# Optimization experiments

Measured on AMD Instinct MI355X. Metric: run time of the kernel, lower is better.

## Reference

```python
import jax, jax.numpy as jnp
import numpy as np
from jax import lax

RADIUS = 4
SIGMA_1 = 5.0
SIGMA_2 = 1.0


def _gaussian_kernel_3d(radius, sigma):
    x = np.linspace(-radius, radius, 2 * radius + 1)
    xx, yy, zz = np.meshgrid(x, x, x)
    dist2 = xx ** 2 + yy ** 2 + zz ** 2
    k = np.exp(-dist2 / (2.0 * sigma ** 2)).astype(np.float32)
    return jnp.asarray(k)[None, None]  # [O=1, I=1, D, H, W]


def _conv3d_same(x, kernel, radius):
    # x: [B,1,D,H,W], kernel: [1,1,kd,kh,kw]
    pad = [(radius, radius)] * 3
    return lax.conv_general_dilated(
        x, kernel, window_strides=(1, 1, 1), padding=pad,
        dimension_numbers=('NCDHW', 'OIDHW', 'NCDHW'))


def setup_inputs() -> dict:
    key = jax.random.key(0)
    k1, k2 = jax.random.split(key)
    labels = jax.random.uniform(k1, (4, 1, 160, 160, 160), dtype=jnp.float32)
    inputs = jax.random.uniform(k2, (4, 1, 160, 160, 160), dtype=jnp.float32)
    return {"labels": labels, "inputs": inputs}


def reference(labels, inputs):
    kernel = _gaussian_kernel_3d(RADIUS, SIGMA_1)
    num_classes = 2
    p0 = labels[:, 0:1]  # [B,1,D,H,W]
    loss = jnp.float32(0.0)
    for k in range(num_classes):
        class_probs = p0 if k == 0 else 1.0 - p0
        class_mean = (jnp.mean(inputs * class_probs, axis=(2, 3, 4), keepdims=True)
                      / (jnp.mean(class_probs, axis=(2, 3, 4), keepdims=True) + 1e-5))
        diff = jnp.sum((inputs - class_mean) ** 2, axis=1, keepdims=True)  # [B,1,D,H,W]
        weights = jnp.exp(-(diff ** 2) / (SIGMA_2 ** 2))
        numerator = jnp.sum(class_probs * _conv3d_same(class_probs * weights, kernel, RADIUS))
        denominator = jnp.sum(class_probs * _conv3d_same(weights, kernel, RADIUS))
        # L1Loss(scalar, 0) == abs(scalar)
        loss = loss + jnp.abs(numerator / (denominator + 1e-6))
    return jnp.float32(num_classes) - loss
```

## Files before the change

### kernel.cpp

```cpp
#include <hip/hip_runtime.h>
#include <hip/hip_fp16.h>
#include <math.h>

#define NX   160
#define N2   25600
#define N3   4096000
#define NB   4

#define NBLK_XY 16000
#define TILES_PER_B 4000
#define NBLK_Z 1600
#define ZCH 10

#define SA_W 52
#define SB_W 36

__device__ __constant__ float G1[9] = {
    0.72614903f, 0.83527021f, 0.92311635f, 0.98019867f, 1.0f,
    0.98019867f, 0.92311635f, 0.83527021f, 0.72614903f};

#define ES_FULL 7.92946852f
__device__ __constant__ float ES_M[4] = {3.46473426f, 2.48453559f, 1.56141924f,
                                         0.72614903f};
__device__ inline float edge_sum(int i) {
    float s = ES_FULL;
    if (i < 4) s -= ES_M[i];
    if (i > NX - 5) s -= ES_M[NX - 1 - i];
    return s;
}

__device__ inline float4 f4_zero() { return make_float4(0.f, 0.f, 0.f, 0.f); }
__device__ inline float4 f4_axpy(float a, float4 b, float4 c) {
    return make_float4(c.x + a * b.x, c.y + a * b.y, c.z + a * b.z, c.w + a * b.w);
}

__device__ inline float4 load_t4(const __half* p) {
    uint2 u = *(const uint2*)p;
    __half2 a = *(const __half2*)&u.x;
    __half2 b = *(const __half2*)&u.y;
    float2 fa = __half22float2(a);
    float2 fb = __half22float2(b);
    return make_float4(fa.x, fa.y, fb.x, fb.y);
}

template <int NV>
__device__ inline void block_reduce_store(double* vals, double* dst) {
    __shared__ double red[4][NV];
    int lane = threadIdx.x & 63;
    int wave = threadIdx.x >> 6;
#pragma unroll
    for (int v = 0; v < NV; ++v) {
        double x = vals[v];
#pragma unroll
        for (int off = 32; off > 0; off >>= 1) x += __shfl_down(x, off, 64);
        if (lane == 0) red[wave][v] = x;
    }
    __syncthreads();
    if (threadIdx.x < NV) {
        int v = threadIdx.x;
        dst[v] = red[0][v] + red[1][v] + red[2][v] + red[3][v];
    }
}

__global__ __launch_bounds__(256) void conv_xy_kernel(
    const float* __restrict__ labels, const float* __restrict__ inputs,
    __half* __restrict__ t, double* __restrict__ pS) {
    __shared__ float sA[40 * SA_W];
    __shared__ float sB[40 * SB_W];

    int bid = blockIdx.x;
    int tileX = bid % 5;
    int tileY = (bid / 5) % 5;
    int zb = bid / 25;
    int sliceOff = zb * N2;
    int x0 = tileX * 32, y0 = tileY * 32;
    int tid = threadIdx.x;

    for (int i = tid; i < 480; i += 256) {
        int row = i / 12, c = i % 12;
        int gx = x0 - 8 + 4 * c;
        int gy = y0 - 4 + row;
        float4 v = f4_zero();
        if (gy >= 0 && gy < NX && gx >= 0 && gx <= NX - 4)
            v = *(const float4*)&labels[sliceOff + gy * NX + gx];
        *(float4*)&sA[row * SA_W + 4 * c] = v;
    }
    __syncthreads();

    for (int i = tid; i < 320; i += 256) {
        int r = i >> 3, x4 = i & 7;
        const float* row = &sA[r * SA_W + 4 * x4];
        float4 a = *(const float4*)&row[4];
        float4 b = *(const float4*)&row[8];
        float4 c = *(const float4*)&row[12];
        float w[12] = {a.x, a.y, a.z, a.w, b.x, b.y, b.z, b.w,
                       c.x, c.y, c.z, c.w};
        float4 o = f4_zero();
#pragma unroll
        for (int d = 0; d < 9; ++d) {
            float g = G1[d];
            o.x += g * w[d];
            o.y += g * w[d + 1];
            o.z += g * w[d + 2];
            o.w += g * w[d + 3];
        }
        *(float4*)&sB[r * SB_W + 4 * x4] = o;
    }
    __syncthreads();

    int oy = tid >> 3, x4 = tid & 7;
    float4 acc = f4_zero();
#pragma unroll
    for (int d = 0; d < 9; ++d) {
        float4 v = *(const float4*)&sB[(oy + d) * SB_W + 4 * x4];
        acc = f4_axpy(G1[d], v, acc);
    }
    int gi = sliceOff + (y0 + oy) * NX + (x0 + 4 * x4);
    __half2 ha = __floats2half2_rn(acc.x, acc.y);
    __half2 hb = __floats2half2_rn(acc.z, acc.w);
    uint2 u;
    u.x = *(unsigned int*)&ha;
    u.y = *(unsigned int*)&hb;
    *(uint2*)&t[gi] = u;

    float4 p = *(const float4*)&sA[(oy + 4) * SA_W + 4 * x4 + 8];
    float4 in = *(const float4*)&inputs[gi];
    double vals[3];
    vals[0] = (double)(p.x + p.y + p.z + p.w);
    vals[1] = (double)(in.x * p.x + in.y * p.y + in.z * p.z + in.w * p.w);
    vals[2] = (double)(in.x + in.y + in.z + in.w);
    block_reduce_store<3>(vals, pS + 3 * bid);
}

__global__ __launch_bounds__(256) void conv_z_kernel(
    const __half* __restrict__ t, const float* __restrict__ labels,
    const float* __restrict__ inputs, const double* __restrict__ pS,
    double* __restrict__ pZ) {
    int tid = threadIdx.x;
    int tidg = blockIdx.x * 256 + tid;
    int x4 = tidg % 40;
    int r = tidg / 40;
    int y = r % NX;
    int zc = (tidg / 6400) % 16;
    int b = tidg / 102400;

    __shared__ double Ssh[3];
    {
        double v0 = 0, v1 = 0, v2 = 0;
        for (int i = tid; i < TILES_PER_B; i += 256) {
            const double* p = pS + 3 * (b * TILES_PER_B + i);
            v0 += p[0]; v1 += p[1]; v2 += p[2];
        }
        double vals[3] = {v0, v1, v2};
        block_reduce_store<3>(vals, Ssh);
        __syncthreads();
    }
    double sp = Ssh[0], sip = Ssh[1], si = Ssh[2];
    const double Nv = (double)N3;
    float m0 = (float)((sip / Nv) / (sp / Nv + 1e-5));
    float m1 = (float)(((si - sip) / Nv) / ((Nv - sp) / Nv + 1e-5));

    int x = x4 * 4;
    float ey = edge_sum(y);
    float cx[4] = {edge_sum(x) * ey, edge_sum(x + 1) * ey,
                   edge_sum(x + 2) * ey, edge_sum(x + 3) * ey};

    int z0 = zc * ZCH;
    int base = b * N3 + y * NX + x;

    float4 win[9];
#pragma unroll
    for (int d = 0; d < 9; ++d) {
        int z = z0 - 4 + d;
        win[d] = (z >= 0 && z < NX) ? load_t4(&t[base + z * N2]) : f4_zero();
    }

    float n0 = 0.f, d0 = 0.f, n1 = 0.f, d1 = 0.f;
#pragma unroll
    for (int g = 0; g < 2; ++g) {
        int zg = z0 + 5 * g;
        float4 tn[5], pv[5], iv[5];
#pragma unroll
        for (int j = 0; j < 5; ++j) {
            int zl = zg + j + 5;
            tn[j] = (zl < NX) ? load_t4(&t[base + zl * N2]) : f4_zero();
            int gi = base + (zg + j) * N2;
            pv[j] = *(const float4*)&labels[gi];
            iv[j] = *(const float4*)&inputs[gi];
        }
#pragma unroll
        for (int j = 0; j < 5; ++j) {
            float4 c4 = f4_zero();
#pragma unroll
            for (int d = 0; d < 9; ++d) c4 = f4_axpy(G1[d], win[d], c4);
            float ez = edge_sum(zg + j);
            float pc[4] = {pv[j].x, pv[j].y, pv[j].z, pv[j].w};
            float ic[4] = {iv[j].x, iv[j].y, iv[j].z, iv[j].w};
            float cc[4] = {c4.x, c4.y, c4.z, c4.w};
#pragma unroll
            for (int l = 0; l < 4; ++l) {
                float c1 = cx[l] * ez - cc[l];
                float df0 = ic[l] - m0; df0 *= df0;
                float w0 = __expf(-df0 * df0);
                float df1 = ic[l] - m1; df1 *= df1;
                float w1 = __expf(-df1 * df1);
                n0 += cc[l] * pc[l] * w0;
                d0 += cc[l] * w0;
                n1 += c1 * (1.f - pc[l]) * w1;
                d1 += c1 * w1;
            }
#pragma unroll
            for (int d = 0; d < 8; ++d) win[d] = win[d + 1];
            win[8] = tn[j];
        }
    }
    double vals[4] = {(double)n0, (double)d0, (double)n1, (double)d1};
    block_reduce_store<4>(vals, pZ + 4 * blockIdx.x);
}

__global__ __launch_bounds__(256) void finalize_kernel(
    const double* __restrict__ pZ, float* __restrict__ out) {
    double a0 = 0, a1 = 0, a2 = 0, a3 = 0;
    for (int i = threadIdx.x; i < NBLK_Z; i += 256) {
        const double* p = &pZ[4 * i];
        a0 += p[0]; a1 += p[1]; a2 += p[2]; a3 += p[3];
    }
    __shared__ double red[4][4];
    int lane = threadIdx.x & 63;
    int wave = threadIdx.x >> 6;
    double vals[4] = {a0, a1, a2, a3};
#pragma unroll
    for (int v = 0; v < 4; ++v) {
        double x = vals[v];
#pragma unroll
        for (int off = 32; off > 0; off >>= 1) x += __shfl_down(x, off, 64);
        if (lane == 0) red[wave][v] = x;
    }
    __syncthreads();
    if (threadIdx.x == 0) {
        double acc[4];
#pragma unroll
        for (int v = 0; v < 4; ++v)
            acc[v] = red[0][v] + red[1][v] + red[2][v] + red[3][v];
        double r0 = fabs(acc[0] / (acc[1] + 1e-6));
        double r1 = fabs(acc[2] / (acc[3] + 1e-6));
        out[0] = (float)(2.0 - r0 - r1);
    }
}

extern "C" void kernel_launch(void* const* d_in, const int* in_sizes, int n_in,
                              void* d_out, int out_size, void* d_ws, size_t ws_size,
                              hipStream_t stream) {
    const float* labels = (const float*)d_in[0];
    const float* inputs = (const float*)d_in[1];
    float* out = (float*)d_out;

    double* pS = (double*)d_ws;
    double* pZ = (double*)((char*)d_ws + 384000);
    __half* t  = (__half*)((char*)d_ws + 524288);

    hipLaunchKernelGGL(conv_xy_kernel, dim3(NBLK_XY), dim3(256), 0, stream,
                       labels, inputs, t, pS);
    hipLaunchKernelGGL(conv_z_kernel, dim3(NBLK_Z), dim3(256), 0, stream,
                       t, labels, inputs, pS, pZ);
    hipLaunchKernelGGL(finalize_kernel, dim3(1), dim3(256), 0, stream, pZ, out);
}
```

Measured before the change: 227.0 us.

## Hoist per-batch mean reduction into separate kernel and shrink z-chunks for parallelism

Moves the per-batch sum reduction of the xy-pass partials out of every conv_z block into a small dedicated 4-block kernel, so each conv_z block no longer rereads 12000 doubles. It also shrinks the z-chunk per thread from 10 to 4 slices, raising the block count from 1600 to 4000. All 12 halo slices and the labels and inputs loads are issued up front. The trade is more redundant halo loads of t (12 slices per 4 outputs instead of 18 per 10) and an extra kernel launch.

```diff
diff --git a/kernel.cpp b/kernel.cpp
--- a/kernel.cpp
+++ b/kernel.cpp
@@ -9,8 +9,8 @@
 
 #define NBLK_XY 16000
 #define TILES_PER_B 4000
-#define NBLK_Z 1600
-#define ZCH 10
+#define ZCH 4
+#define NBLK_Z 4000
 
 #define SA_W 52
 #define SB_W 36
@@ -34,13 +34,21 @@
     return make_float4(c.x + a * b.x, c.y + a * b.y, c.z + a * b.z, c.w + a * b.w);
 }
 
-__device__ inline float4 load_t4(const __half* p) {
-    uint2 u = *(const uint2*)p;
+__device__ inline float4 h4_decode(uint2 u) {
     __half2 a = *(const __half2*)&u.x;
     __half2 b = *(const __half2*)&u.y;
     float2 fa = __half22float2(a);
     float2 fb = __half22float2(b);
     return make_float4(fa.x, fa.y, fb.x, fb.y);
+}
+
+__device__ inline uint2 h4_encode(float4 v) {
+    __half2 a = __floats2half2_rn(v.x, v.y);
+    __half2 b = __floats2half2_rn(v.z, v.w);
+    uint2 u;
+    u.x = *(unsigned int*)&a;
+    u.y = *(unsigned int*)&b;
+    return u;
 }
 
 template <int NV>
@@ -116,12 +124,7 @@
         acc = f4_axpy(G1[d], v, acc);
     }
     int gi = sliceOff + (y0 + oy) * NX + (x0 + 4 * x4);
-    __half2 ha = __floats2half2_rn(acc.x, acc.y);
-    __half2 hb = __floats2half2_rn(acc.z, acc.w);
-    uint2 u;
-    u.x = *(unsigned int*)&ha;
-    u.y = *(unsigned int*)&hb;
-    *(uint2*)&t[gi] = u;
+    *(uint2*)&t[gi] = h4_encode(acc);
 
     float4 p = *(const float4*)&sA[(oy + 4) * SA_W + 4 * x4 + 8];
     float4 in = *(const float4*)&inputs[gi];
@@ -132,30 +135,30 @@
     block_reduce_store<3>(vals, pS + 3 * bid);
 }
 
+__global__ __launch_bounds__(256) void reduce_S_kernel(
+    const double* __restrict__ pS, double* __restrict__ S) {
+    int b = blockIdx.x;
+    double v0 = 0, v1 = 0, v2 = 0;
+    for (int i = threadIdx.x; i < TILES_PER_B; i += 256) {
+        const double* p = pS + 3 * (b * TILES_PER_B + i);
+        v0 += p[0]; v1 += p[1]; v2 += p[2];
+    }
+    double vals[3] = {v0, v1, v2};
+    block_reduce_store<3>(vals, S + 3 * b);
+}
+
 __global__ __launch_bounds__(256) void conv_z_kernel(
     const __half* __restrict__ t, const float* __restrict__ labels,
-    const float* __restrict__ inputs, const double* __restrict__ pS,
+    const float* __restrict__ inputs, const double* __restrict__ S,
     double* __restrict__ pZ) {
     int tid = threadIdx.x;
     int tidg = blockIdx.x * 256 + tid;
     int x4 = tidg % 40;
-    int r = tidg / 40;
-    int y = r % NX;
-    int zc = (tidg / 6400) % 16;
-    int b = tidg / 102400;
-
-    __shared__ double Ssh[3];
-    {
-        double v0 = 0, v1 = 0, v2 = 0;
-        for (int i = tid; i < TILES_PER_B; i += 256) {
-            const double* p = pS + 3 * (b * TILES_PER_B + i);
-            v0 += p[0]; v1 += p[1]; v2 += p[2];
-        }
-        double vals[3] = {v0, v1, v2};
-        block_reduce_store<3>(vals, Ssh);
-        __syncthreads();
-    }
-    double sp = Ssh[0], sip = Ssh[1], si = Ssh[2];
+    int y = (tidg / 40) % NX;
+    int zc = (tidg / 6400) % 40;
+    int b = tidg / 256000;
+
+    double sp = S[3 * b + 0], sip = S[3 * b + 1], si = S[3 * b + 2];
     const double Nv = (double)N3;
     float m0 = (float)((sip / Nv) / (sp / Nv + 1e-5));
     float m1 = (float)(((si - sip) / Nv) / ((Nv - sp) / Nv + 1e-5));
@@ -168,50 +171,46 @@
     int z0 = zc * ZCH;
     int base = b * N3 + y * NX + x;
 
-    float4 win[9];
-#pragma unroll
-    for (int d = 0; d < 9; ++d) {
+    uint2 tr[12];
+#pragma unroll
+    for (int d = 0; d < 12; ++d) {
         int z = z0 - 4 + d;
-        win[d] = (z >= 0 && z < NX) ? load_t4(&t[base + z * N2]) : f4_zero();
-    }
+        tr[d] = (z >= 0 && z < NX) ? *(const uint2*)&t[base + z * N2]
+                                   : make_uint2(0u, 0u);
+    }
+    float4 pv[4], iv[4];
+#pragma unroll
+    for (int j = 0; j < 4; ++j) {
+        int gi = base + (z0 + j) * N2;
+        pv[j] = *(const float4*)&labels[gi];
+        iv[j] = *(const float4*)&inputs[gi];
+    }
+
+    float4 tw[12];
+#pragma unroll
+    for (int d = 0; d < 12; ++d) tw[d] = h4_decode(tr[d]);
 
     float n0 = 0.f, d0 = 0.f, n1 = 0.f, d1 = 0.f;
 #pragma unroll
-    for (int g = 0; g < 2; ++g) {
-        int zg = z0 + 5 * g;
-        float4 tn[5], pv[5], iv[5];
-#pragma unroll
-        for (int j = 0; j < 5; ++j) {
-            int zl = zg + j + 5;
-            tn[j] = (zl < NX) ? load_t4(&t[base + zl * N2]) : f4_zero();
-            int gi = base + (zg + j) * N2;
-            pv[j] = *(const float4*)&labels[gi];
-            iv[j] = *(const float4*)&inputs[gi];
-        }
-#pragma unroll
-        for (int j = 0; j < 5; ++j) {
-            float4 c4 = f4_zero();
-#pragma unroll
-            for (int d = 0; d < 9; ++d) c4 = f4_axpy(G1[d], win[d], c4);
-            float ez = edge_sum(zg + j);
-            float pc[4] = {pv[j].x, pv[j].y, pv[j].z, pv[j].w};
-            float ic[4] = {iv[j].x, iv[j].y, iv[j].z, iv[j].w};
-            float cc[4] = {c4.x, c4.y, c4.z, c4.w};
-#pragma unroll
-            for (int l = 0; l < 4; ++l) {
-                float c1 = cx[l] * ez - cc[l];
-                float df0 = ic[l] - m0; df0 *= df0;
-                float w0 = __expf(-df0 * df0);
-                float df1 = ic[l] - m1; df1 *= df1;
-                float w1 = __expf(-df1 * df1);
-                n0 += cc[l] * pc[l] * w0;
-                d0 += cc[l] * w0;
-                n1 += c1 * (1.f - pc[l]) * w1;
-                d1 += c1 * w1;
-            }
-#pragma unroll
-            for (int d = 0; d < 8; ++d) win[d] = win[d + 1];
-            win[8] = tn[j];
+    for (int j = 0; j < 4; ++j) {
+        float4 c4 = f4_zero();
+#pragma unroll
+        for (int d = 0; d < 9; ++d) c4 = f4_axpy(G1[d], tw[j + d], c4);
+        float ez = edge_sum(z0 + j);
+        float pc[4] = {pv[j].x, pv[j].y, pv[j].z, pv[j].w};
+        float ic[4] = {iv[j].x, iv[j].y, iv[j].z, iv[j].w};
+        float cc[4] = {c4.x, c4.y, c4.z, c4.w};
+#pragma unroll
+        for (int l = 0; l < 4; ++l) {
+            float c1 = cx[l] * ez - cc[l];
+            float df0 = ic[l] - m0; df0 *= df0;
+            float w0 = __expf(-df0 * df0);
+            float df1 = ic[l] - m1; df1 *= df1;
+            float w1 = __expf(-df1 * df1);
+            n0 += cc[l] * pc[l] * w0;
+            d0 += cc[l] * w0;
+            n1 += c1 * (1.f - pc[l]) * w1;
+            d1 += c1 * w1;
         }
     }
     double vals[4] = {(double)n0, (double)d0, (double)n1, (double)d1};
@@ -256,12 +255,14 @@
     float* out = (float*)d_out;
 
     double* pS = (double*)d_ws;
-    double* pZ = (double*)((char*)d_ws + 384000);
+    double* S  = (double*)((char*)d_ws + 384000);
+    double* pZ = (double*)((char*)d_ws + 384096);
     __half* t  = (__half*)((char*)d_ws + 524288);
 
     hipLaunchKernelGGL(conv_xy_kernel, dim3(NBLK_XY), dim3(256), 0, stream,
                        labels, inputs, t, pS);
+    hipLaunchKernelGGL(reduce_S_kernel, dim3(NB), dim3(256), 0, stream, pS, S);
     hipLaunchKernelGGL(conv_z_kernel, dim3(NBLK_Z), dim3(256), 0, stream,
-                       t, labels, inputs, pS, pZ);
+                       t, labels, inputs, S, pZ);
     hipLaunchKernelGGL(finalize_kernel, dim3(1), dim3(256), 0, stream, pZ, out);
 }
```

Result: faster. 208.7 us (-8.1%).
